# Optimization experiments

Measured on AMD Instinct MI355X. Metric: run time of the kernel, lower is better.

The kernel has to match this reference:

```python
import jax, jax.numpy as jnp
import numpy as np

V, D, NL, NC = 16, 256, 4, 2
MAXL, NSTATE, DCONV, EXPAND, HEADDIM = 1024, 64, 4, 2, 64
DIN = EXPAND * D            # 512 inner channels
H = DIN // HEADDIM          # 8 heads
P = HEADDIM                 # 64 head dim
CONV_DIM = DIN + 2 * NSTATE # 640 channels through depthwise conv
D_IN_PROJ = 2 * DIN + 2 * NSTATE + H  # 1160
B_, L_ = 2, 1024
EPS = 1e-5


def setup_inputs() -> dict:
    key = jax.random.key(0)
    ks = iter(jax.random.split(key, 32))

    def rn(shape, s=0.02):
        return jax.random.normal(next(ks), shape, jnp.float32) * s

    emb = rn((V, D)).at[4].set(0.0)  # padding_idx=4 row zeroed
    pos_emb = rn((MAXL, D))
    in_proj_w = rn((NL, D_IN_PROJ, D))
    conv_w = rn((NL, CONV_DIM, DCONV), 0.1)
    conv_b = rn((NL, CONV_DIM), 0.1)
    dt_bias = rn((NL, H), 0.5)
    A_log = jnp.log(jax.random.uniform(next(ks), (NL, H), jnp.float32, 1.0, 16.0))
    D_param = jnp.ones((NL, H), jnp.float32)
    norm_w = jnp.ones((NL, DIN), jnp.float32)
    out_proj_w = rn((NL, D, DIN))
    pooler_w = rn((D, D), 0.05)
    pooler_b = jnp.zeros((D,), jnp.float32)
    cls1_w = rn((D // 2, D), 0.05)
    cls1_b = jnp.zeros((D // 2,), jnp.float32)
    cls2_w = rn((NC, D // 2), 0.05)
    cls2_b = jnp.zeros((NC,), jnp.float32)
    input_ids = jax.random.randint(next(ks), (B_, L_), 0, V)
    return dict(input_ids=input_ids, emb=emb, pos_emb=pos_emb,
                in_proj_w=in_proj_w, conv_w=conv_w, conv_b=conv_b,
                dt_bias=dt_bias, A_log=A_log, D_param=D_param, norm_w=norm_w,
                out_proj_w=out_proj_w, pooler_w=pooler_w, pooler_b=pooler_b,
                cls1_w=cls1_w, cls1_b=cls1_b, cls2_w=cls2_w, cls2_b=cls2_b)


def _mamba2(x, Win, cw, cb, dtb, A_log, Dp, nw, Wout):
    Bsz, L, _ = x.shape
    zxbcdt = jnp.einsum('bld,pd->blp', x, Win)              # (B,L,2*DIN+2N+H)
    z = zxbcdt[..., :DIN]
    xBC = zxbcdt[..., DIN:DIN + CONV_DIM]
    dt = jax.nn.softplus(zxbcdt[..., -H:] + dtb)            # (B,L,H)
    # causal depthwise conv over time
    xBC = jnp.transpose(xBC, (0, 2, 1))                     # (B,C,L)
    xBC = jax.lax.conv_general_dilated(
        xBC, cw[:, None, :], (1,), [(DCONV - 1, 0)],
        dimension_numbers=('NCH', 'OIH', 'NCH'),
        feature_group_count=CONV_DIM)
    xBC = jax.nn.silu(jnp.transpose(xBC, (0, 2, 1)) + cb)   # (B,L,C)
    xs = xBC[..., :DIN].reshape(Bsz, L, H, P)
    Bm = xBC[..., DIN:DIN + NSTATE]                         # (B,L,N)
    Cm = xBC[..., DIN + NSTATE:]                            # (B,L,N)
    A = -jnp.exp(A_log)                                     # (H,)
    dA = jnp.exp(dt * A)                                    # (B,L,H)
    dBx = dt[..., None, None] * xs[..., None] * Bm[:, :, None, None, :]  # (B,L,H,P,N)

    def step(h, inp):
        dA_t, dBx_t, C_t = inp
        h = dA_t[:, :, None, None] * h + dBx_t              # (B,H,P,N)
        y = jnp.einsum('bhpn,bn->bhp', h, C_t)
        return h, y

    h0 = jnp.zeros((Bsz, H, P, NSTATE), x.dtype)
    _, y = jax.lax.scan(step, h0, (jnp.moveaxis(dA, 1, 0),
                                   jnp.moveaxis(dBx, 1, 0),
                                   jnp.moveaxis(Cm, 1, 0)))
    y = jnp.moveaxis(y, 0, 1) + Dp[None, None, :, None] * xs  # (B,L,H,P)
    y = y.reshape(Bsz, L, DIN) * jax.nn.silu(z)               # gated
    y = y * jax.lax.rsqrt(jnp.mean(y * y, axis=-1, keepdims=True) + EPS) * nw
    return jnp.einsum('bld,od->blo', y, Wout)


def reference(input_ids, emb, pos_emb, in_proj_w, conv_w, conv_b, dt_bias,
              A_log, D_param, norm_w, out_proj_w, pooler_w, pooler_b,
              cls1_w, cls1_b, cls2_w, cls2_b):
    L = input_ids.shape[1]
    x = emb[input_ids] + pos_emb[:L][None]                  # (B,L,D)
    for i in range(NL):
        x = x + _mamba2(x, in_proj_w[i], conv_w[i], conv_b[i], dt_bias[i],
                        A_log[i], D_param[i], norm_w[i], out_proj_w[i])
    pooled = (x.mean(axis=1) + x.max(axis=1)) * 0.5         # (B,D)
    pooled = jax.nn.gelu(pooled @ pooler_w.T + pooler_b, approximate=False)
    hcls = jax.nn.gelu(pooled @ cls1_w.T + cls1_b, approximate=False)
    return hcls @ cls2_w.T + cls2_b
```

## Files before the change

### kernel.cpp

```cpp
#include <hip/hip_runtime.h>
#include <math.h>

#define D_ 256
#define NL_ 4
#define NC_ 2
#define L_LEN 1024
#define NSTATE_ 64
#define DIN_ 512
#define H_ 8
#define P_ 64
#define CONVDIM_ 640
#define DPROJ_ 1160
#define EPS_ 1e-5f
#define NCH_ 16

typedef __attribute__((ext_vector_type(8))) short short8;
typedef __attribute__((ext_vector_type(4))) float f32x4;
typedef __attribute__((ext_vector_type(4))) unsigned short us4;

__device__ __forceinline__ float siluf(float x) { return x / (1.f + __expf(-x)); }
__device__ __forceinline__ float geluf(float x) { return 0.5f * x * (1.f + erff(x * 0.70710678118654752f)); }
__device__ __forceinline__ unsigned short f2bf(float f) {
    unsigned u = __float_as_uint(f);
    u += 0x7FFFu + ((u >> 16) & 1u);
    return (unsigned short)(u >> 16);
}
__device__ __forceinline__ float bf2f(unsigned short h) {
    return __uint_as_float(((unsigned)h) << 16);
}

__global__ void k_embed(const int* __restrict__ ids, const float* __restrict__ emb,
                        const float* __restrict__ pos, float* __restrict__ x, int total) {
    int i = blockIdx.x * blockDim.x + threadIdx.x;
    if (i >= total) return;
    int d = i & (D_ - 1);
    int bl = i >> 8;
    int l = bl & (L_LEN - 1);
    x[i] = emb[ids[bl] * D_ + d] + pos[l * D_ + d];
}

__global__ void k_w2bf(const float* __restrict__ W, unsigned short* __restrict__ hi,
                       unsigned short* __restrict__ lo, int n) {
    int i = blockIdx.x * blockDim.x + threadIdx.x;
    if (i >= n) return;
    float f = W[i];
    unsigned short h = f2bf(f);
    hi[i] = h;
    lo[i] = f2bf(f - bf2f(h));
}

template <bool ATOMIC>
__global__ void __launch_bounds__(256) gemm_bf3(const float* __restrict__ A,
        const unsigned short* __restrict__ Bhi, const unsigned short* __restrict__ Blo,
        float* __restrict__ C, int M, int N, int K, int kchunk) {
    __shared__ __align__(16) unsigned short Ah[128 * 40];
    __shared__ __align__(16) unsigned short Al[128 * 40];
    __shared__ __align__(16) unsigned short Bh[64 * 40];
    __shared__ __align__(16) unsigned short Bl[64 * 40];
    const int tid = threadIdx.x;
    const int col0 = blockIdx.x * 64;
    const int row0 = blockIdx.y * 128;
    const int kbase = blockIdx.z * kchunk;

    const int sar = tid >> 1, sas = (tid & 1) * 16;
    const int sbr = tid >> 2, sbs = (tid & 3) * 8;
    const bool bok = (col0 + sbr) < N;
    const float* aptr = A + (size_t)(row0 + sar) * K + kbase + sas;
    const unsigned short* bhptr = Bhi + (size_t)(col0 + sbr) * K + kbase + sbs;
    const unsigned short* blptr = Blo + (size_t)(col0 + sbr) * K + kbase + sbs;

    float4 pa[4];
    short8 pbh = {0, 0, 0, 0, 0, 0, 0, 0}, pbl = {0, 0, 0, 0, 0, 0, 0, 0};
#pragma unroll
    for (int i = 0; i < 4; ++i) pa[i] = *(const float4*)(aptr + i * 4);
    if (bok) {
        pbh = *(const short8*)bhptr;
        pbl = *(const short8*)blptr;
    }

    const int wave = tid >> 6, lane = tid & 63;
    const int lq = lane >> 4, lm = lane & 15;
    f32x4 acc[2][4] = {};
    const int nsteps = kchunk >> 5;
    for (int s = 0; s < nsteps; ++s) {
        __syncthreads();
#pragma unroll
        for (int i = 0; i < 4; ++i) {
            float4 f = pa[i];
            unsigned short h0 = f2bf(f.x), h1 = f2bf(f.y), h2 = f2bf(f.z), h3 = f2bf(f.w);
            us4 hv = {h0, h1, h2, h3};
            us4 lv = {f2bf(f.x - bf2f(h0)), f2bf(f.y - bf2f(h1)),
                      f2bf(f.z - bf2f(h2)), f2bf(f.w - bf2f(h3))};
            *(us4*)&Ah[sar * 40 + sas + i * 4] = hv;
            *(us4*)&Al[sar * 40 + sas + i * 4] = lv;
        }
        *(short8*)&Bh[sbr * 40 + sbs] = pbh;
        *(short8*)&Bl[sbr * 40 + sbs] = pbl;
        __syncthreads();
        if (s + 1 < nsteps) {
            int ko = (s + 1) * 32;
#pragma unroll
            for (int i = 0; i < 4; ++i) pa[i] = *(const float4*)(aptr + ko + i * 4);
            if (bok) {
                pbh = *(const short8*)(bhptr + ko);
                pbl = *(const short8*)(blptr + ko);
            }
        }
        short8 bh[4], bl[4];
#pragma unroll
        for (int ct = 0; ct < 4; ++ct) {
            bh[ct] = *(const short8*)&Bh[(ct * 16 + lm) * 40 + lq * 8];
            bl[ct] = *(const short8*)&Bl[(ct * 16 + lm) * 40 + lq * 8];
        }
#pragma unroll
        for (int rt = 0; rt < 2; ++rt) {
            short8 ah = *(const short8*)&Ah[(wave * 32 + rt * 16 + lm) * 40 + lq * 8];
            short8 al = *(const short8*)&Al[(wave * 32 + rt * 16 + lm) * 40 + lq * 8];
#pragma unroll
            for (int ct = 0; ct < 4; ++ct) {
                acc[rt][ct] = __builtin_amdgcn_mfma_f32_16x16x32_bf16(ah, bh[ct], acc[rt][ct], 0, 0, 0);
                acc[rt][ct] = __builtin_amdgcn_mfma_f32_16x16x32_bf16(ah, bl[ct], acc[rt][ct], 0, 0, 0);
                acc[rt][ct] = __builtin_amdgcn_mfma_f32_16x16x32_bf16(al, bh[ct], acc[rt][ct], 0, 0, 0);
            }
        }
    }
#pragma unroll
    for (int rt = 0; rt < 2; ++rt) {
#pragma unroll
        for (int ct = 0; ct < 4; ++ct) {
            int col = col0 + ct * 16 + lm;
            if (col >= N) continue;
            int rbase = row0 + wave * 32 + rt * 16 + lq * 4;
#pragma unroll
            for (int reg = 0; reg < 4; ++reg) {
                size_t idx = (size_t)(rbase + reg) * N + col;
                if (ATOMIC) atomicAdd(&C[idx], acc[rt][ct][reg]);
                else C[idx] = acc[rt][ct][reg];
            }
        }
    }
}

__global__ void __launch_bounds__(256) k_ssmA(const float* __restrict__ zx,
        const float* __restrict__ cw, const float* __restrict__ cb,
        const float* __restrict__ dtbias, const float* __restrict__ Alog,
        const float* __restrict__ Dp,
        float* __restrict__ Sbuf, float* __restrict__ decay,
        float* __restrict__ Ctil, float* __restrict__ y) {
    __shared__ float U[64][65];
    __shared__ float V[64][65];
    __shared__ float W[64][65];
    __shared__ float sdt[64], cs[64], wj[64];
    const int c = blockIdx.x, bh = blockIdx.y;
    const int b = bh >> 3, h = bh & 7;
    const int l0 = c << 6;
    const int tid = threadIdx.x, wid = tid >> 6, lane = tid & 63;

    const int chx = h * P_ + lane;
    const int chb = DIN_ + lane;
    const int chc = DIN_ + NSTATE_ + lane;
    float wx0 = cw[chx * 4], wx1 = cw[chx * 4 + 1], wx2 = cw[chx * 4 + 2], wx3 = cw[chx * 4 + 3];
    float wb0 = cw[chb * 4], wb1 = cw[chb * 4 + 1], wb2 = cw[chb * 4 + 2], wb3 = cw[chb * 4 + 3];
    float wc0 = cw[chc * 4], wc1 = cw[chc * 4 + 1], wc2 = cw[chc * 4 + 2], wc3 = cw[chc * 4 + 3];
    float bx = cb[chx], bb = cb[chb], bc = cb[chc];

    for (int r = 0; r < 64; r += 4) {
        int j = r + wid;
        int l = l0 + j;
        float ax = bx, ab = bb, ac = bc;
#pragma unroll
        for (int k = 0; k < 4; ++k) {
            int t = l - 3 + k;
            if (t >= 0) {
                const float* row = zx + (size_t)(b * L_LEN + t) * DPROJ_;
                float wxk = (k == 0) ? wx0 : (k == 1) ? wx1 : (k == 2) ? wx2 : wx3;
                float wbk = (k == 0) ? wb0 : (k == 1) ? wb1 : (k == 2) ? wb2 : wb3;
                float wck = (k == 0) ? wc0 : (k == 1) ? wc1 : (k == 2) ? wc2 : wc3;
                ax += wxk * row[DIN_ + chx];
                ab += wbk * row[DIN_ + chb];
                ac += wck * row[DIN_ + chc];
            }
        }
        U[j][lane] = siluf(ax);
        V[j][lane] = siluf(ab);
        W[j][lane] = siluf(ac);
    }
    if (tid < 64) {
        float xv = zx[(size_t)(b * L_LEN + l0 + tid) * DPROJ_ + (DPROJ_ - H_) + h] + dtbias[h];
        float sp = fmaxf(xv, 0.f) + log1pf(__expf(-fabsf(xv)));
        sdt[tid] = sp;
        cs[tid] = sp * (-__expf(Alog[h]));
    }
    __syncthreads();
    if (tid == 0) {
        float s = 0.f;
        for (int j = 0; j < 64; ++j) { s += cs[j]; cs[j] = s; }
    }
    __syncthreads();
    if (tid < 64) wj[tid] = __expf(cs[63] - cs[tid]) * sdt[tid];
    if (tid == 0) decay[bh * NCH_ + c] = __expf(cs[63]);
    __syncthreads();

    const int t4 = (tid & 15) * 4;
    const int r4 = (tid >> 4) * 4;
    const size_t sbase = (size_t)(bh * NCH_ + c) * 4096;

    {
        float acc[4][4] = {};
        for (int j = 0; j < 64; ++j) {
            float w = wj[j];
            float4 xv = *(const float4*)&U[j][r4];
            float4 bv = *(const float4*)&V[j][t4];
            float xw[4] = {xv.x * w, xv.y * w, xv.z * w, xv.w * w};
#pragma unroll
            for (int ii = 0; ii < 4; ++ii) {
                acc[ii][0] += xw[ii] * bv.x;
                acc[ii][1] += xw[ii] * bv.y;
                acc[ii][2] += xw[ii] * bv.z;
                acc[ii][3] += xw[ii] * bv.w;
            }
        }
#pragma unroll
        for (int ii = 0; ii < 4; ++ii) {
            float4 v = {acc[ii][0], acc[ii][1], acc[ii][2], acc[ii][3]};
            *(float4*)&Sbuf[sbase + (size_t)(r4 + ii) * 64 + t4] = v;
        }
    }
    for (int r = 0; r < 64; r += 4) {
        int ii = r + wid;
        Ctil[sbase + ii * 64 + lane] = __expf(cs[ii]) * W[ii][lane];
    }
    float g[4][4] = {};
    for (int ng = 0; ng < 64; ng += 4) {
        float4 cf[4], bf[4];
#pragma unroll
        for (int ii = 0; ii < 4; ++ii) cf[ii] = *(const float4*)&W[r4 + ii][ng];
#pragma unroll
        for (int jj = 0; jj < 4; ++jj) bf[jj] = *(const float4*)&V[t4 + jj][ng];
#pragma unroll
        for (int ii = 0; ii < 4; ++ii)
#pragma unroll
            for (int jj = 0; jj < 4; ++jj)
                g[ii][jj] += cf[ii].x * bf[jj].x + cf[ii].y * bf[jj].y +
                             cf[ii].z * bf[jj].z + cf[ii].w * bf[jj].w;
    }
    float wt[4][4];
#pragma unroll
    for (int ii = 0; ii < 4; ++ii) {
        int i = r4 + ii;
        float csi = cs[i];
#pragma unroll
        for (int jj = 0; jj < 4; ++jj) {
            int j = t4 + jj;
            wt[ii][jj] = (j <= i) ? __expf(fminf(csi - cs[j], 0.f)) * sdt[j] * g[ii][jj] : 0.f;
        }
    }
    __syncthreads();
#pragma unroll
    for (int jj = 0; jj < 4; ++jj) {
        float4 v = {wt[0][jj], wt[1][jj], wt[2][jj], wt[3][jj]};
        *(float4*)&V[t4 + jj][r4] = v;
    }
    __syncthreads();
    {
        float acc[4][4] = {};
        for (int j = 0; j < 64; ++j) {
            float4 wv = *(const float4*)&V[j][r4];
            float4 xv = *(const float4*)&U[j][t4];
            float ws[4] = {wv.x, wv.y, wv.z, wv.w};
#pragma unroll
            for (int ii = 0; ii < 4; ++ii) {
                acc[ii][0] += ws[ii] * xv.x;
                acc[ii][1] += ws[ii] * xv.y;
                acc[ii][2] += ws[ii] * xv.z;
                acc[ii][3] += ws[ii] * xv.w;
            }
        }
        float Dh = Dp[h];
#pragma unroll
        for (int ii = 0; ii < 4; ++ii) {
            float4 xv = *(const float4*)&U[r4 + ii][t4];
            float4 v = {acc[ii][0] + Dh * xv.x, acc[ii][1] + Dh * xv.y,
                        acc[ii][2] + Dh * xv.z, acc[ii][3] + Dh * xv.w};
            *(float4*)&y[(size_t)(b * L_LEN + l0 + r4 + ii) * DIN_ + h * P_ + t4] = v;
        }
    }
}

__global__ void __launch_bounds__(256) k_inter(const float* __restrict__ Sbuf,
        const float* __restrict__ Ctil, const float* __restrict__ decay,
        float* __restrict__ y) {
    __shared__ float Sm[64][65];
    __shared__ float Cm[64][65];
    const int c = blockIdx.x + 1, bh = blockIdx.y;
    const int b = bh >> 3, h = bh & 7;
    const int l0 = c << 6;
    const int tid = threadIdx.x, wid = tid >> 6, lane = tid & 63;
    const size_t bhbase = (size_t)bh * NCH_ * 4096;

    float dec[NCH_];
#pragma unroll
    for (int k = 0; k < NCH_; ++k) dec[k] = decay[bh * NCH_ + k];

    float acc16[16] = {};
    float wgt = 1.f;
    for (int cp = c - 1; cp >= 0; --cp) {
        const float* src = Sbuf + bhbase + (size_t)cp * 4096;
#pragma unroll
        for (int i = 0; i < 16; ++i) acc16[i] += wgt * src[i * 256 + tid];
        wgt *= dec[cp];
    }
#pragma unroll
    for (int i = 0; i < 16; ++i) Sm[i * 4 + wid][lane] = acc16[i];

    const size_t base = bhbase + (size_t)c * 4096;
    for (int r = 0; r < 64; r += 4) {
        int pp = r + wid;
        Cm[pp][lane] = Ctil[base + pp * 64 + lane];
    }
    __syncthreads();
    const int t4 = (tid & 15) * 4;
    const int r4 = (tid >> 4) * 4;
    float acc[4][4] = {};
    for (int ng = 0; ng < 64; ng += 4) {
        float4 cf[4], sf[4];
#pragma unroll
        for (int ii = 0; ii < 4; ++ii) cf[ii] = *(const float4*)&Cm[r4 + ii][ng];
#pragma unroll
        for (int pp = 0; pp < 4; ++pp) sf[pp] = *(const float4*)&Sm[t4 + pp][ng];
#pragma unroll
        for (int ii = 0; ii < 4; ++ii)
#pragma unroll
            for (int pp = 0; pp < 4; ++pp)
                acc[ii][pp] += cf[ii].x * sf[pp].x + cf[ii].y * sf[pp].y +
                               cf[ii].z * sf[pp].z + cf[ii].w * sf[pp].w;
    }
#pragma unroll
    for (int ii = 0; ii < 4; ++ii) {
        float* dst = &y[(size_t)(b * L_LEN + l0 + r4 + ii) * DIN_ + h * P_ + t4];
        float4 v = *(const float4*)dst;
        v.x += acc[ii][0]; v.y += acc[ii][1]; v.z += acc[ii][2]; v.w += acc[ii][3];
        *(float4*)dst = v;
    }
}

__global__ void k_gatenorm(const float* __restrict__ zx, const float* __restrict__ nw,
                           float* __restrict__ y) {
    __shared__ float sred[4];
    int bl = blockIdx.x;
    float* yr = y + (size_t)bl * DIN_;
    const float* zr = zx + (size_t)bl * DPROJ_;
    int t = threadIdx.x;
    float g0 = yr[t] * siluf(zr[t]);
    float g1 = yr[t + 256] * siluf(zr[t + 256]);
    float ss = g0 * g0 + g1 * g1;
#pragma unroll
    for (int o = 32; o; o >>= 1) ss += __shfl_xor(ss, o, 64);
    if ((t & 63) == 0) sred[t >> 6] = ss;
    __syncthreads();
    ss = sred[0] + sred[1] + sred[2] + sred[3];
    float scale = rsqrtf(ss * (1.f / DIN_) + EPS_);
    yr[t] = g0 * scale * nw[t];
    yr[t + 256] = g1 * scale * nw[t + 256];
}

__global__ void k_pool1(const float* __restrict__ x, float* __restrict__ psum,
                        float* __restrict__ pmax) {
    int b = blockIdx.y, ch = blockIdx.x, d = threadIdx.x;
    const float* xb = x + ((size_t)(b * L_LEN) + ch * 64) * D_ + d;
    float s = 0.f, m = -INFINITY;
    for (int l = 0; l < 64; ++l) {
        float v = xb[(size_t)l * D_];
        s += v;
        m = fmaxf(m, v);
    }
    psum[(b * 16 + ch) * D_ + d] = s;
    pmax[(b * 16 + ch) * D_ + d] = m;
}

__global__ void k_poolhead(const float* __restrict__ psum, const float* __restrict__ pmax,
                           const float* __restrict__ pw, const float* __restrict__ pb,
                           const float* __restrict__ c1w, const float* __restrict__ c1b,
                           const float* __restrict__ c2w, const float* __restrict__ c2b,
                           float* __restrict__ out) {
    __shared__ float sp[256], s1[256], s2[128];
    int b = blockIdx.x, t = threadIdx.x;
    float s = 0.f, m = -INFINITY;
    for (int ch = 0; ch < 16; ++ch) {
        s += psum[(b * 16 + ch) * D_ + t];
        m = fmaxf(m, pmax[(b * 16 + ch) * D_ + t]);
    }
    sp[t] = (s * (1.f / L_LEN) + m) * 0.5f;
    __syncthreads();
    float acc = pb[t];
    for (int d = 0; d < 256; ++d) acc += sp[d] * pw[t * 256 + d];
    s1[t] = geluf(acc);
    __syncthreads();
    if (t < 128) {
        float a = c1b[t];
        for (int d = 0; d < 256; ++d) a += s1[d] * c1w[t * 256 + d];
        s2[t] = geluf(a);
    }
    __syncthreads();
    if (t < 2) {
        float a = c2b[t];
        for (int d = 0; d < 128; ++d) a += s2[d] * c2w[t * 128 + d];
        out[b * NC_ + t] = a;
    }
}

extern "C" void kernel_launch(void* const* d_in, const int* in_sizes, int n_in,
                              void* d_out, int out_size, void* d_ws, size_t ws_size,
                              hipStream_t stream) {
    const int* ids    = (const int*)d_in[0];
    const float* emb  = (const float*)d_in[1];
    const float* pos  = (const float*)d_in[2];
    const float* Wins = (const float*)d_in[3];
    const float* cw   = (const float*)d_in[4];
    const float* cb   = (const float*)d_in[5];
    const float* dtb  = (const float*)d_in[6];
    const float* Alog = (const float*)d_in[7];
    const float* Dpar = (const float*)d_in[8];
    const float* nw   = (const float*)d_in[9];
    const float* Wout = (const float*)d_in[10];
    const float* pw   = (const float*)d_in[11];
    const float* pb   = (const float*)d_in[12];
    const float* c1w  = (const float*)d_in[13];
    const float* c1b  = (const float*)d_in[14];
    const float* c2w  = (const float*)d_in[15];
    const float* c2b  = (const float*)d_in[16];
    float* out = (float*)d_out;

    const int NWIN = NL_ * DPROJ_ * D_;
    const int NWOUT = NL_ * D_ * DIN_;

    float* ws = (float*)d_ws;
    float* x      = ws;
    float* zx     = x + 524288;
    float* y      = zx + 2375680;
    float* Sbuf   = y + 1048576;
    float* Ctil   = Sbuf + 1048576;
    float* decay  = Ctil + 1048576;
    float* psum   = decay + 256;
    float* pmax   = psum + 8192;
    unsigned short* winh = (unsigned short*)(pmax + 8192);
    unsigned short* winl = winh + NWIN;
    unsigned short* woh  = winl + NWIN;
    unsigned short* wol  = woh + NWOUT;

    k_w2bf<<<(NWIN + 255) / 256, 256, 0, stream>>>(Wins, winh, winl, NWIN);
    k_w2bf<<<(NWOUT + 255) / 256, 256, 0, stream>>>(Wout, woh, wol, NWOUT);
    k_embed<<<2048, 256, 0, stream>>>(ids, emb, pos, x, 524288);
    for (int i = 0; i < NL_; ++i) {
        size_t wo_in = (size_t)i * DPROJ_ * D_;
        size_t wo_out = (size_t)i * D_ * DIN_;
        gemm_bf3<false><<<dim3(19, 16, 1), 256, 0, stream>>>(
            x, winh + wo_in, winl + wo_in, zx, 2048, DPROJ_, D_, D_);
        k_ssmA<<<dim3(NCH_, 16), 256, 0, stream>>>(
            zx, cw + (size_t)i * CONVDIM_ * 4, cb + (size_t)i * CONVDIM_,
            dtb + i * H_, Alog + i * H_, Dpar + i * H_, Sbuf, decay, Ctil, y);
        k_inter<<<dim3(NCH_ - 1, 16), 256, 0, stream>>>(Sbuf, Ctil, decay, y);
        k_gatenorm<<<2048, 256, 0, stream>>>(zx, nw + (size_t)i * DIN_, y);
        gemm_bf3<true><<<dim3(4, 16, 4), 256, 0, stream>>>(
            y, woh + wo_out, wol + wo_out, x, 2048, D_, DIN_, 128);
    }
    k_pool1<<<dim3(16, 2), 256, 0, stream>>>(x, psum, pmax);
    k_poolhead<<<2, 256, 0, stream>>>(psum, pmax, pw, pb, c1w, c1b, c2w, c2b, out);
}
```

Before: 417.5 us.

## Fuse gated RMSNorm into out-projection GEMM and double SSM block threads

The gate-and-normalise pass is split into a small row-scale kernel that only computes the per-row RMS factor. The silu gating, scaling and norm weight are now applied while the output-projection GEMM loads its A tile, so the normalised activations are never written back to memory. The SSM intra-chunk and inter-chunk kernels move from 256 to 512 threads, with each thread handling 2 rows instead of 4 to raise parallelism, and the two weight-conversion launches are merged into one. The cost is recomputing silu once per column-block in the GEMM (four times per element) and giving up some per-thread register reuse in the SSM kernels.

```diff
diff --git a/kernel.cpp b/kernel.cpp
--- a/kernel.cpp
+++ b/kernel.cpp
@@ -39,17 +39,26 @@
     x[i] = emb[ids[bl] * D_ + d] + pos[l * D_ + d];
 }
 
-__global__ void k_w2bf(const float* __restrict__ W, unsigned short* __restrict__ hi,
-                       unsigned short* __restrict__ lo, int n) {
+__global__ void k_w2bf2(const float* __restrict__ Wi, const float* __restrict__ Wo,
+                        unsigned short* __restrict__ wih, unsigned short* __restrict__ wil,
+                        unsigned short* __restrict__ woh, unsigned short* __restrict__ wol,
+                        int nin, int ntot) {
     int i = blockIdx.x * blockDim.x + threadIdx.x;
-    if (i >= n) return;
-    float f = W[i];
-    unsigned short h = f2bf(f);
-    hi[i] = h;
-    lo[i] = f2bf(f - bf2f(h));
-}
-
-template <bool ATOMIC>
+    if (i >= ntot) return;
+    if (i < nin) {
+        float f = Wi[i];
+        unsigned short h = f2bf(f);
+        wih[i] = h;
+        wil[i] = f2bf(f - bf2f(h));
+    } else {
+        int j = i - nin;
+        float f = Wo[j];
+        unsigned short h = f2bf(f);
+        woh[j] = h;
+        wol[j] = f2bf(f - bf2f(h));
+    }
+}
+
 __global__ void __launch_bounds__(256) gemm_bf3(const float* __restrict__ A,
         const unsigned short* __restrict__ Bhi, const unsigned short* __restrict__ Blo,
         float* __restrict__ C, int M, int N, int K, int kchunk) {
@@ -134,14 +143,133 @@
 #pragma unroll
             for (int reg = 0; reg < 4; ++reg) {
                 size_t idx = (size_t)(rbase + reg) * N + col;
-                if (ATOMIC) atomicAdd(&C[idx], acc[rt][ct][reg]);
-                else C[idx] = acc[rt][ct][reg];
-            }
-        }
-    }
-}
-
-__global__ void __launch_bounds__(256) k_ssmA(const float* __restrict__ zx,
+                C[idx] = acc[rt][ct][reg];
+            }
+        }
+    }
+}
+
+__global__ void __launch_bounds__(256) k_rowscale(const float* __restrict__ y,
+        const float* __restrict__ zx, float* __restrict__ scale) {
+    int row = blockIdx.x * 4 + (threadIdx.x >> 6);
+    int lane = threadIdx.x & 63;
+    const float* yr = y + (size_t)row * DIN_ + lane * 8;
+    const float* zr = zx + (size_t)row * DPROJ_ + lane * 8;
+    float4 y0 = *(const float4*)yr, y1 = *(const float4*)(yr + 4);
+    float4 z0 = *(const float4*)zr, z1 = *(const float4*)(zr + 4);
+    float g;
+    float ss = 0.f;
+    g = y0.x * siluf(z0.x); ss += g * g;
+    g = y0.y * siluf(z0.y); ss += g * g;
+    g = y0.z * siluf(z0.z); ss += g * g;
+    g = y0.w * siluf(z0.w); ss += g * g;
+    g = y1.x * siluf(z1.x); ss += g * g;
+    g = y1.y * siluf(z1.y); ss += g * g;
+    g = y1.z * siluf(z1.z); ss += g * g;
+    g = y1.w * siluf(z1.w); ss += g * g;
+#pragma unroll
+    for (int o = 32; o; o >>= 1) ss += __shfl_xor(ss, o, 64);
+    if (lane == 0) scale[row] = rsqrtf(ss * (1.f / DIN_) + EPS_);
+}
+
+__global__ void __launch_bounds__(256) gemm_outg3(const float* __restrict__ y,
+        const float* __restrict__ zx, const float* __restrict__ nw,
+        const float* __restrict__ scale,
+        const unsigned short* __restrict__ Bhi, const unsigned short* __restrict__ Blo,
+        float* __restrict__ x) {
+    __shared__ __align__(16) unsigned short Ah[128 * 40];
+    __shared__ __align__(16) unsigned short Al[128 * 40];
+    __shared__ __align__(16) unsigned short Bh[64 * 40];
+    __shared__ __align__(16) unsigned short Bl[64 * 40];
+    const int tid = threadIdx.x;
+    const int col0 = blockIdx.x * 64;
+    const int row0 = blockIdx.y * 128;
+    const int kbase = blockIdx.z * 128;
+    const int sar = tid >> 1, sas = (tid & 1) * 16;
+    const int sbr = tid >> 2, sbs = (tid & 3) * 8;
+    const float* yp = y + (size_t)(row0 + sar) * DIN_ + kbase + sas;
+    const float* zp = zx + (size_t)(row0 + sar) * DPROJ_ + kbase + sas;
+    const unsigned short* bhptr = Bhi + (size_t)(col0 + sbr) * DIN_ + kbase + sbs;
+    const unsigned short* blptr = Blo + (size_t)(col0 + sbr) * DIN_ + kbase + sbs;
+    const float sc = scale[row0 + sar];
+
+    float4 py[4], pz[4], pnw[4];
+    short8 pbh, pbl;
+#pragma unroll
+    for (int i = 0; i < 4; ++i) {
+        py[i] = *(const float4*)(yp + i * 4);
+        pz[i] = *(const float4*)(zp + i * 4);
+        pnw[i] = *(const float4*)&nw[kbase + sas + i * 4];
+    }
+    pbh = *(const short8*)bhptr;
+    pbl = *(const short8*)blptr;
+
+    const int wave = tid >> 6, lane = tid & 63;
+    const int lq = lane >> 4, lm = lane & 15;
+    f32x4 acc[2][4] = {};
+    for (int s = 0; s < 4; ++s) {
+        __syncthreads();
+#pragma unroll
+        for (int i = 0; i < 4; ++i) {
+            float4 fy = py[i], fz = pz[i], fn = pnw[i];
+            float g0 = fy.x * siluf(fz.x) * sc * fn.x;
+            float g1 = fy.y * siluf(fz.y) * sc * fn.y;
+            float g2 = fy.z * siluf(fz.z) * sc * fn.z;
+            float g3 = fy.w * siluf(fz.w) * sc * fn.w;
+            unsigned short h0 = f2bf(g0), h1 = f2bf(g1), h2 = f2bf(g2), h3 = f2bf(g3);
+            us4 hv = {h0, h1, h2, h3};
+            us4 lv = {f2bf(g0 - bf2f(h0)), f2bf(g1 - bf2f(h1)),
+                      f2bf(g2 - bf2f(h2)), f2bf(g3 - bf2f(h3))};
+            *(us4*)&Ah[sar * 40 + sas + i * 4] = hv;
+            *(us4*)&Al[sar * 40 + sas + i * 4] = lv;
+        }
+        *(short8*)&Bh[sbr * 40 + sbs] = pbh;
+        *(short8*)&Bl[sbr * 40 + sbs] = pbl;
+        __syncthreads();
+        if (s + 1 < 4) {
+            int ko = (s + 1) * 32;
+#pragma unroll
+            for (int i = 0; i < 4; ++i) {
+                py[i] = *(const float4*)(yp + ko + i * 4);
+                pz[i] = *(const float4*)(zp + ko + i * 4);
+                pnw[i] = *(const float4*)&nw[kbase + ko + sas + i * 4];
+            }
+            pbh = *(const short8*)(bhptr + ko);
+            pbl = *(const short8*)(blptr + ko);
+        }
+        short8 bh[4], bl[4];
+#pragma unroll
+        for (int ct = 0; ct < 4; ++ct) {
+            bh[ct] = *(const short8*)&Bh[(ct * 16 + lm) * 40 + lq * 8];
+            bl[ct] = *(const short8*)&Bl[(ct * 16 + lm) * 40 + lq * 8];
+        }
+#pragma unroll
+        for (int rt = 0; rt < 2; ++rt) {
+            short8 ah = *(const short8*)&Ah[(wave * 32 + rt * 16 + lm) * 40 + lq * 8];
+            short8 al = *(const short8*)&Al[(wave * 32 + rt * 16 + lm) * 40 + lq * 8];
+#pragma unroll
+            for (int ct = 0; ct < 4; ++ct) {
+                acc[rt][ct] = __builtin_amdgcn_mfma_f32_16x16x32_bf16(ah, bh[ct], acc[rt][ct], 0, 0, 0);
+                acc[rt][ct] = __builtin_amdgcn_mfma_f32_16x16x32_bf16(ah, bl[ct], acc[rt][ct], 0, 0, 0);
+                acc[rt][ct] = __builtin_amdgcn_mfma_f32_16x16x32_bf16(al, bh[ct], acc[rt][ct], 0, 0, 0);
+            }
+        }
+    }
+#pragma unroll
+    for (int rt = 0; rt < 2; ++rt) {
+#pragma unroll
+        for (int ct = 0; ct < 4; ++ct) {
+            int col = col0 + ct * 16 + lm;
+            int rbase = row0 + wave * 32 + rt * 16 + lq * 4;
+#pragma unroll
+            for (int reg = 0; reg < 4; ++reg) {
+                atomicAdd(&x[(size_t)(rbase + reg) * D_ + col], acc[rt][ct][reg]);
+            }
+        }
+    }
+}
+
+__global__ void __launch_bounds__(512) k_ssmA(const float* __restrict__ zx,
         const float* __restrict__ cw, const float* __restrict__ cb,
         const float* __restrict__ dtbias, const float* __restrict__ Alog,
         const float* __restrict__ Dp,
@@ -154,7 +282,7 @@
     const int c = blockIdx.x, bh = blockIdx.y;
     const int b = bh >> 3, h = bh & 7;
     const int l0 = c << 6;
-    const int tid = threadIdx.x, wid = tid >> 6, lane = tid & 63;
+    const int tid = threadIdx.x, wid8 = tid >> 6, lane = tid & 63;
 
     const int chx = h * P_ + lane;
     const int chb = DIN_ + lane;
@@ -164,8 +292,8 @@
     float wc0 = cw[chc * 4], wc1 = cw[chc * 4 + 1], wc2 = cw[chc * 4 + 2], wc3 = cw[chc * 4 + 3];
     float bx = cb[chx], bb = cb[chb], bc = cb[chc];
 
-    for (int r = 0; r < 64; r += 4) {
-        int j = r + wid;
+    for (int r = 0; r < 64; r += 8) {
+        int j = r + wid8;
         int l = l0 + j;
         float ax = bx, ab = bb, ac = bc;
 #pragma unroll
@@ -201,53 +329,46 @@
     if (tid == 0) decay[bh * NCH_ + c] = __expf(cs[63]);
     __syncthreads();
 
+    const int r2 = (tid >> 4) * 2;
     const int t4 = (tid & 15) * 4;
-    const int r4 = (tid >> 4) * 4;
     const size_t sbase = (size_t)(bh * NCH_ + c) * 4096;
 
     {
-        float acc[4][4] = {};
+        float acc[2][4] = {};
         for (int j = 0; j < 64; ++j) {
             float w = wj[j];
-            float4 xv = *(const float4*)&U[j][r4];
+            float x0 = U[j][r2] * w, x1 = U[j][r2 + 1] * w;
             float4 bv = *(const float4*)&V[j][t4];
-            float xw[4] = {xv.x * w, xv.y * w, xv.z * w, xv.w * w};
-#pragma unroll
-            for (int ii = 0; ii < 4; ++ii) {
-                acc[ii][0] += xw[ii] * bv.x;
-                acc[ii][1] += xw[ii] * bv.y;
-                acc[ii][2] += xw[ii] * bv.z;
-                acc[ii][3] += xw[ii] * bv.w;
-            }
-        }
-#pragma unroll
-        for (int ii = 0; ii < 4; ++ii) {
+            acc[0][0] += x0 * bv.x; acc[0][1] += x0 * bv.y;
+            acc[0][2] += x0 * bv.z; acc[0][3] += x0 * bv.w;
+            acc[1][0] += x1 * bv.x; acc[1][1] += x1 * bv.y;
+            acc[1][2] += x1 * bv.z; acc[1][3] += x1 * bv.w;
+        }
+#pragma unroll
+        for (int ii = 0; ii < 2; ++ii) {
             float4 v = {acc[ii][0], acc[ii][1], acc[ii][2], acc[ii][3]};
-            *(float4*)&Sbuf[sbase + (size_t)(r4 + ii) * 64 + t4] = v;
-        }
-    }
-    for (int r = 0; r < 64; r += 4) {
-        int ii = r + wid;
+            *(float4*)&Sbuf[sbase + (size_t)(r2 + ii) * 64 + t4] = v;
+        }
+    }
+    for (int r = 0; r < 64; r += 8) {
+        int ii = r + wid8;
         Ctil[sbase + ii * 64 + lane] = __expf(cs[ii]) * W[ii][lane];
     }
-    float g[4][4] = {};
+    float g[2][4] = {};
     for (int ng = 0; ng < 64; ng += 4) {
-        float4 cf[4], bf[4];
-#pragma unroll
-        for (int ii = 0; ii < 4; ++ii) cf[ii] = *(const float4*)&W[r4 + ii][ng];
-#pragma unroll
-        for (int jj = 0; jj < 4; ++jj) bf[jj] = *(const float4*)&V[t4 + jj][ng];
-#pragma unroll
-        for (int ii = 0; ii < 4; ++ii)
-#pragma unroll
-            for (int jj = 0; jj < 4; ++jj)
-                g[ii][jj] += cf[ii].x * bf[jj].x + cf[ii].y * bf[jj].y +
-                             cf[ii].z * bf[jj].z + cf[ii].w * bf[jj].w;
-    }
-    float wt[4][4];
-#pragma unroll
-    for (int ii = 0; ii < 4; ++ii) {
-        int i = r4 + ii;
+        float4 cf0 = *(const float4*)&W[r2][ng];
+        float4 cf1 = *(const float4*)&W[r2 + 1][ng];
+#pragma unroll
+        for (int jj = 0; jj < 4; ++jj) {
+            float4 bf = *(const float4*)&V[t4 + jj][ng];
+            g[0][jj] += cf0.x * bf.x + cf0.y * bf.y + cf0.z * bf.z + cf0.w * bf.w;
+            g[1][jj] += cf1.x * bf.x + cf1.y * bf.y + cf1.z * bf.z + cf1.w * bf.w;
+        }
+    }
+    float wt[2][4];
+#pragma unroll
+    for (int ii = 0; ii < 2; ++ii) {
+        int i = r2 + ii;
         float csi = cs[i];
 #pragma unroll
         for (int jj = 0; jj < 4; ++jj) {
@@ -258,36 +379,32 @@
     __syncthreads();
 #pragma unroll
     for (int jj = 0; jj < 4; ++jj) {
-        float4 v = {wt[0][jj], wt[1][jj], wt[2][jj], wt[3][jj]};
-        *(float4*)&V[t4 + jj][r4] = v;
+        V[t4 + jj][r2] = wt[0][jj];
+        V[t4 + jj][r2 + 1] = wt[1][jj];
     }
     __syncthreads();
     {
-        float acc[4][4] = {};
+        float acc[2][4] = {};
         for (int j = 0; j < 64; ++j) {
-            float4 wv = *(const float4*)&V[j][r4];
+            float w0 = V[j][r2], w1 = V[j][r2 + 1];
             float4 xv = *(const float4*)&U[j][t4];
-            float ws[4] = {wv.x, wv.y, wv.z, wv.w};
-#pragma unroll
-            for (int ii = 0; ii < 4; ++ii) {
-                acc[ii][0] += ws[ii] * xv.x;
-                acc[ii][1] += ws[ii] * xv.y;
-                acc[ii][2] += ws[ii] * xv.z;
-                acc[ii][3] += ws[ii] * xv.w;
-            }
+            acc[0][0] += w0 * xv.x; acc[0][1] += w0 * xv.y;
+            acc[0][2] += w0 * xv.z; acc[0][3] += w0 * xv.w;
+            acc[1][0] += w1 * xv.x; acc[1][1] += w1 * xv.y;
+            acc[1][2] += w1 * xv.z; acc[1][3] += w1 * xv.w;
         }
         float Dh = Dp[h];
 #pragma unroll
-        for (int ii = 0; ii < 4; ++ii) {
-            float4 xv = *(const float4*)&U[r4 + ii][t4];
+        for (int ii = 0; ii < 2; ++ii) {
+            float4 xv = *(const float4*)&U[r2 + ii][t4];
             float4 v = {acc[ii][0] + Dh * xv.x, acc[ii][1] + Dh * xv.y,
                         acc[ii][2] + Dh * xv.z, acc[ii][3] + Dh * xv.w};
-            *(float4*)&y[(size_t)(b * L_LEN + l0 + r4 + ii) * DIN_ + h * P_ + t4] = v;
-        }
-    }
-}
-
-__global__ void __launch_bounds__(256) k_inter(const float* __restrict__ Sbuf,
+            *(float4*)&y[(size_t)(b * L_LEN + l0 + r2 + ii) * DIN_ + h * P_ + t4] = v;
+        }
+    }
+}
+
+__global__ void __launch_bounds__(512) k_inter(const float* __restrict__ Sbuf,
         const float* __restrict__ Ctil, const float* __restrict__ decay,
         float* __restrict__ y) {
     __shared__ float Sm[64][65];
@@ -295,73 +412,50 @@
     const int c = blockIdx.x + 1, bh = blockIdx.y;
     const int b = bh >> 3, h = bh & 7;
     const int l0 = c << 6;
-    const int tid = threadIdx.x, wid = tid >> 6, lane = tid & 63;
+    const int tid = threadIdx.x, wid8 = tid >> 6, lane = tid & 63;
     const size_t bhbase = (size_t)bh * NCH_ * 4096;
 
     float dec[NCH_];
 #pragma unroll
     for (int k = 0; k < NCH_; ++k) dec[k] = decay[bh * NCH_ + k];
 
-    float acc16[16] = {};
+    float acc8[8] = {};
     float wgt = 1.f;
     for (int cp = c - 1; cp >= 0; --cp) {
         const float* src = Sbuf + bhbase + (size_t)cp * 4096;
 #pragma unroll
-        for (int i = 0; i < 16; ++i) acc16[i] += wgt * src[i * 256 + tid];
+        for (int i = 0; i < 8; ++i) acc8[i] += wgt * src[i * 512 + tid];
         wgt *= dec[cp];
     }
 #pragma unroll
-    for (int i = 0; i < 16; ++i) Sm[i * 4 + wid][lane] = acc16[i];
+    for (int i = 0; i < 8; ++i) Sm[i * 8 + wid8][lane] = acc8[i];
 
     const size_t base = bhbase + (size_t)c * 4096;
-    for (int r = 0; r < 64; r += 4) {
-        int pp = r + wid;
+    for (int r = 0; r < 64; r += 8) {
+        int pp = r + wid8;
         Cm[pp][lane] = Ctil[base + pp * 64 + lane];
     }
     __syncthreads();
+    const int r2 = (tid >> 4) * 2;
     const int t4 = (tid & 15) * 4;
-    const int r4 = (tid >> 4) * 4;
-    float acc[4][4] = {};
+    float acc[2][4] = {};
     for (int ng = 0; ng < 64; ng += 4) {
-        float4 cf[4], sf[4];
-#pragma unroll
-        for (int ii = 0; ii < 4; ++ii) cf[ii] = *(const float4*)&Cm[r4 + ii][ng];
-#pragma unroll
-        for (int pp = 0; pp < 4; ++pp) sf[pp] = *(const float4*)&Sm[t4 + pp][ng];
-#pragma unroll
-        for (int ii = 0; ii < 4; ++ii)
-#pragma unroll
-            for (int pp = 0; pp < 4; ++pp)
-                acc[ii][pp] += cf[ii].x * sf[pp].x + cf[ii].y * sf[pp].y +
-                               cf[ii].z * sf[pp].z + cf[ii].w * sf[pp].w;
-    }
-#pragma unroll
-    for (int ii = 0; ii < 4; ++ii) {
-        float* dst = &y[(size_t)(b * L_LEN + l0 + r4 + ii) * DIN_ + h * P_ + t4];
+        float4 cf0 = *(const float4*)&Cm[r2][ng];
+        float4 cf1 = *(const float4*)&Cm[r2 + 1][ng];
+#pragma unroll
+        for (int pp = 0; pp < 4; ++pp) {
+            float4 sf = *(const float4*)&Sm[t4 + pp][ng];
+            acc[0][pp] += cf0.x * sf.x + cf0.y * sf.y + cf0.z * sf.z + cf0.w * sf.w;
+            acc[1][pp] += cf1.x * sf.x + cf1.y * sf.y + cf1.z * sf.z + cf1.w * sf.w;
+        }
+    }
+#pragma unroll
+    for (int ii = 0; ii < 2; ++ii) {
+        float* dst = &y[(size_t)(b * L_LEN + l0 + r2 + ii) * DIN_ + h * P_ + t4];
         float4 v = *(const float4*)dst;
         v.x += acc[ii][0]; v.y += acc[ii][1]; v.z += acc[ii][2]; v.w += acc[ii][3];
         *(float4*)dst = v;
     }
-}
-
-__global__ void k_gatenorm(const float* __restrict__ zx, const float* __restrict__ nw,
-                           float* __restrict__ y) {
-    __shared__ float sred[4];
-    int bl = blockIdx.x;
-    float* yr = y + (size_t)bl * DIN_;
-    const float* zr = zx + (size_t)bl * DPROJ_;
-    int t = threadIdx.x;
-    float g0 = yr[t] * siluf(zr[t]);
-    float g1 = yr[t + 256] * siluf(zr[t + 256]);
-    float ss = g0 * g0 + g1 * g1;
-#pragma unroll
-    for (int o = 32; o; o >>= 1) ss += __shfl_xor(ss, o, 64);
-    if ((t & 63) == 0) sred[t >> 6] = ss;
-    __syncthreads();
-    ss = sred[0] + sred[1] + sred[2] + sred[3];
-    float scale = rsqrtf(ss * (1.f / DIN_) + EPS_);
-    yr[t] = g0 * scale * nw[t];
-    yr[t + 256] = g1 * scale * nw[t + 256];
 }
 
 __global__ void k_pool1(const float* __restrict__ x, float* __restrict__ psum,
@@ -443,26 +537,27 @@
     float* decay  = Ctil + 1048576;
     float* psum   = decay + 256;
     float* pmax   = psum + 8192;
-    unsigned short* winh = (unsigned short*)(pmax + 8192);
+    float* rscale = pmax + 8192;
+    unsigned short* winh = (unsigned short*)(rscale + 2048);
     unsigned short* winl = winh + NWIN;
     unsigned short* woh  = winl + NWIN;
     unsigned short* wol  = woh + NWOUT;
 
-    k_w2bf<<<(NWIN + 255) / 256, 256, 0, stream>>>(Wins, winh, winl, NWIN);
-    k_w2bf<<<(NWOUT + 255) / 256, 256, 0, stream>>>(Wout, woh, wol, NWOUT);
+    k_w2bf2<<<(NWIN + NWOUT + 255) / 256, 256, 0, stream>>>(
+        Wins, Wout, winh, winl, woh, wol, NWIN, NWIN + NWOUT);
     k_embed<<<2048, 256, 0, stream>>>(ids, emb, pos, x, 524288);
     for (int i = 0; i < NL_; ++i) {
         size_t wo_in = (size_t)i * DPROJ_ * D_;
         size_t wo_out = (size_t)i * D_ * DIN_;
-        gemm_bf3<false><<<dim3(19, 16, 1), 256, 0, stream>>>(
+        gemm_bf3<<<dim3(19, 16, 1), 256, 0, stream>>>(
             x, winh + wo_in, winl + wo_in, zx, 2048, DPROJ_, D_, D_);
-        k_ssmA<<<dim3(NCH_, 16), 256, 0, stream>>>(
+        k_ssmA<<<dim3(NCH_, 16), 512, 0, stream>>>(
             zx, cw + (size_t)i * CONVDIM_ * 4, cb + (size_t)i * CONVDIM_,
             dtb + i * H_, Alog + i * H_, Dpar + i * H_, Sbuf, decay, Ctil, y);
-        k_inter<<<dim3(NCH_ - 1, 16), 256, 0, stream>>>(Sbuf, Ctil, decay, y);
-        k_gatenorm<<<2048, 256, 0, stream>>>(zx, nw + (size_t)i * DIN_, y);
-        gemm_bf3<true><<<dim3(4, 16, 4), 256, 0, stream>>>(
-            y, woh + wo_out, wol + wo_out, x, 2048, D_, DIN_, 128);
+        k_inter<<<dim3(NCH_ - 1, 16), 512, 0, stream>>>(Sbuf, Ctil, decay, y);
+        k_rowscale<<<512, 256, 0, stream>>>(y, zx, rscale);
+        gemm_outg3<<<dim3(4, 16, 4), 256, 0, stream>>>(
+            y, zx, nw + (size_t)i * DIN_, rscale, woh + wo_out, wol + wo_out, x);
     }
     k_pool1<<<dim3(16, 2), 256, 0, stream>>>(x, psum, pmax);
     k_poolhead<<<2, 256, 0, stream>>>(psum, pmax, pw, pb, c1w, c1b, c2w, c2b, out);
```

Result: slower. 571.0 us (+36.8%).
